# Optimization experiments

Measured on AMD Instinct MI355X. Metric: run time of the kernel, lower is better.

## Reference

```python
import jax, jax.numpy as jnp
import numpy as np

QUERY_DIM, FEAT_DIM, HID_DIM, OUT_DIM = 512, 2048, 512, 512
B, L, S, T = 8, 128, 100, 100


def setup_inputs() -> dict:
    key = jax.random.key(0)
    ks = jax.random.split(key, 9)
    d = {
        "query": jax.random.normal(ks[0], (B, L, QUERY_DIM), jnp.float32),
        "src": jax.random.normal(ks[1], (B, S, FEAT_DIM), jnp.float32),
        "trg": jax.random.normal(ks[2], (B, T, FEAT_DIM), jnp.float32),
        # params (LinearAct == Linear + identity act); src/trg projections share weights
        "Wq": jax.random.normal(ks[3], (QUERY_DIM, HID_DIM), jnp.float32) / np.sqrt(QUERY_DIM),
        "bq": jnp.zeros((HID_DIM,), jnp.float32),
        "Ws": jax.random.normal(ks[4], (FEAT_DIM, HID_DIM), jnp.float32) / np.sqrt(FEAT_DIM),
        "bs": jnp.zeros((HID_DIM,), jnp.float32),
        "Wo": jax.random.normal(ks[5], (HID_DIM + QUERY_DIM, OUT_DIM), jnp.float32) / np.sqrt(HID_DIM + QUERY_DIM),
        "bo": jnp.zeros((OUT_DIM,), jnp.float32),
    }
    return d


def reference(query, src, trg, Wq, bq, Ws, bs, Wo, bo):
    b, l, _ = query.shape
    s = src.shape[1]
    t = trg.shape[1]
    q = query @ Wq + bq          # b,l,k
    s_key = src @ Ws + bs        # b,s,k
    t_key = trg @ Ws + bs        # b,t,k
    hid = q.shape[-1]
    # score[b,l,s,t] = q . (s_key - t_key)/sqrt(2) / sqrt(hid) -- decomposed, no b,s,t,k tensor
    qs = jnp.einsum('blk,bsk->bls', q, s_key)
    qt = jnp.einsum('blk,btk->blt', q, t_key)
    score = (qs[:, :, :, None] - qt[:, :, None, :]) / jnp.sqrt(jnp.asarray(2.0 * hid, q.dtype))
    w = jax.nn.softmax(score.reshape(b, l, s * t), axis=-1).reshape(b, l, s, t)
    # ctx = sum_{s,t} w * (s_key - t_key)/sqrt(2), decomposed via marginals
    ws = w.sum(axis=3)           # b,l,s
    wt = w.sum(axis=2)           # b,l,t
    ctx = (jnp.einsum('bls,bsk->blk', ws, s_key) - jnp.einsum('blt,btk->blk', wt, t_key)) / jnp.sqrt(jnp.asarray(2.0, q.dtype))
    x = jnp.concatenate([query, ctx], axis=-1) @ Wo + bo
    return x
```

## Files before the change

### kernel.cpp

```cpp
#include <hip/hip_runtime.h>
#include <math.h>


typedef __attribute__((ext_vector_type(8))) short s16x8;
typedef __attribute__((ext_vector_type(4))) float f32x4;

__device__ __forceinline__ unsigned short f2bf(float f) {
    unsigned int u = __float_as_uint(f);
    return (unsigned short)((u + 0x7fffu + ((u >> 16) & 1u)) >> 16);
}

__device__ __forceinline__ s16x8 cvt8(const float* p) {
    float4 u = *(const float4*)p, w = *(const float4*)(p + 4);
    s16x8 o;
    o[0] = (short)f2bf(u.x); o[1] = (short)f2bf(u.y);
    o[2] = (short)f2bf(u.z); o[3] = (short)f2bf(u.w);
    o[4] = (short)f2bf(w.x); o[5] = (short)f2bf(w.y);
    o[6] = (short)f2bf(w.z); o[7] = (short)f2bf(w.w);
    return o;
}

__global__ __launch_bounds__(256) void k_prep(
    const float* __restrict__ Wq, const float* __restrict__ Ws,
    const float* __restrict__ Wo, const float* __restrict__ bs,
    unsigned short* __restrict__ WqT, unsigned short* __restrict__ WsT,
    unsigned short* __restrict__ WoT, float* __restrict__ keys) {
    __shared__ float tile[32][33];
    const int bid = blockIdx.x, t = threadIdx.x;

    if (bid < 1792) {
        const int id = bid;
        const float* W; unsigned short* O; int K, tk, tn;
        if (id < 256)       { W = Wq; O = WqT; K = 512;  tk = id >> 4;          tn = id & 15; }
        else if (id < 1280) { W = Ws; O = WsT; K = 2048; tk = (id - 256) >> 4;  tn = (id - 256) & 15; }
        else                { W = Wo; O = WoT; K = 1024; tk = (id - 1280) >> 4; tn = (id - 1280) & 15; }
        const int row = t >> 3, c4 = (t & 7) * 4;
        float4 v = *(const float4*)(W + (size_t)(tk * 32 + row) * 512 + tn * 32 + c4);
        tile[row][c4 + 0] = v.x; tile[row][c4 + 1] = v.y;
        tile[row][c4 + 2] = v.z; tile[row][c4 + 3] = v.w;
        __syncthreads();
        ushort4 o = make_ushort4(f2bf(tile[c4 + 0][row]), f2bf(tile[c4 + 1][row]),
                                 f2bf(tile[c4 + 2][row]), f2bf(tile[c4 + 3][row]));
        *(ushort4*)(O + (size_t)(tn * 32 + row) * K + tk * 32 + c4) = o;
    } else {
        const int f = ((bid - 1792) * 256 + t) * 4;
        *(float4*)(keys + f) = *(const float4*)(bs + (f & 511));
    }
}

__device__ __forceinline__ void gemm64_keys(
    const float* __restrict__ src, const float* __restrict__ trg,
    const unsigned short* __restrict__ BT, float* __restrict__ C,
    int m0, int n0, int kbase, unsigned short* As, unsigned short* Bs) {
    const int t = threadIdx.x;
    const int lane = t & 63, wid = t >> 6;
    const int wm = (wid & 1) * 32, wn = (wid >> 1) * 32;
    const int lr = lane & 15, lq = lane >> 4;
    const int r = t >> 3, c8 = (t & 7) * 8;

    const int ra_row = m0 + r, rb_row = m0 + r + 32;
    const float* arp = (ra_row < 800) ? (src + (size_t)ra_row * 2048)
                                      : (trg + (size_t)(ra_row - 800) * 2048);
    const float* brp = (rb_row < 800) ? (src + (size_t)rb_row * 2048)
                                      : (trg + (size_t)(rb_row - 800) * 2048);

    s16x8 ra0, ra1, rb0, rb1;
#define LDK(kt)                                                            \
    ra0 = cvt8(arp + (kt) + c8);                                           \
    ra1 = cvt8(brp + (kt) + c8);                                           \
    rb0 = *(const s16x8*)(BT + (size_t)(n0 + r)      * 2048 + (kt) + c8);  \
    rb1 = *(const s16x8*)(BT + (size_t)(n0 + r + 32) * 2048 + (kt) + c8);

    f32x4 acc[2][2] = {};
    LDK(kbase);
    for (int it = 0; it < 16; it++) {
        __syncthreads();
        *(s16x8*)&As[r * 72 + c8]        = ra0;
        *(s16x8*)&As[(r + 32) * 72 + c8] = ra1;
        *(s16x8*)&Bs[r * 72 + c8]        = rb0;
        *(s16x8*)&Bs[(r + 32) * 72 + c8] = rb1;
        __syncthreads();
        if (it < 15) { LDK(kbase + (it + 1) * 64); }
#pragma unroll
        for (int s = 0; s < 2; s++) {
            s16x8 a0 = *(const s16x8*)&As[(wm + lr) * 72      + s * 32 + lq * 8];
            s16x8 a1 = *(const s16x8*)&As[(wm + 16 + lr) * 72 + s * 32 + lq * 8];
            s16x8 b0 = *(const s16x8*)&Bs[(wn + lr) * 72      + s * 32 + lq * 8];
            s16x8 b1 = *(const s16x8*)&Bs[(wn + 16 + lr) * 72 + s * 32 + lq * 8];
            acc[0][0] = __builtin_amdgcn_mfma_f32_16x16x32_bf16(a0, b0, acc[0][0], 0, 0, 0);
            acc[0][1] = __builtin_amdgcn_mfma_f32_16x16x32_bf16(a0, b1, acc[0][1], 0, 0, 0);
            acc[1][0] = __builtin_amdgcn_mfma_f32_16x16x32_bf16(a1, b0, acc[1][0], 0, 0, 0);
            acc[1][1] = __builtin_amdgcn_mfma_f32_16x16x32_bf16(a1, b1, acc[1][1], 0, 0, 0);
        }
    }
#undef LDK
#pragma unroll
    for (int i = 0; i < 2; i++)
#pragma unroll
        for (int j = 0; j < 2; j++) {
            const int col = n0 + wn + j * 16 + lr;
            const int row = m0 + wm + i * 16 + lq * 4;
#pragma unroll
            for (int rr = 0; rr < 4; rr++)
                unsafeAtomicAdd(&C[(size_t)(row + rr) * 512 + col], acc[i][j][rr]);
        }
}

template <int MODE, bool AF32>
__device__ __forceinline__ void gemm32(
    const void* __restrict__ Av, const unsigned short* __restrict__ BT,
    const float* __restrict__ bias, void* __restrict__ Cv,
    int m0, int n0, int KA, int KB, int N, int kbase, int kiters,
    unsigned short* As, unsigned short* Bs) {
    const int t = threadIdx.x;
    const int lane = t & 63, wid = t >> 6;
    const int wm = (wid & 1) * 16, wn = (wid >> 1) * 32;
    const int lr = lane & 15, lq = lane >> 4;
    const int r = t >> 3, c8 = (t & 7) * 8;
    const float* Af = (const float*)Av;
    const unsigned short* Ab = (const unsigned short*)Av;

    s16x8 ra, rb0, rb1;
#define LD32(kt)                                                                 \
    ra  = AF32 ? cvt8(Af + (size_t)(m0 + r) * KA + (kt) + c8)                    \
               : *(const s16x8*)(Ab + (size_t)(m0 + r) * KA + (kt) + c8);        \
    rb0 = *(const s16x8*)(BT + (size_t)(n0 + r)      * KB + (kt) + c8);          \
    rb1 = *(const s16x8*)(BT + (size_t)(n0 + r + 32) * KB + (kt) + c8);

    f32x4 acc[2] = {};
    LD32(kbase);
    for (int it = 0; it < kiters; it++) {
        __syncthreads();
        *(s16x8*)&As[r * 72 + c8]        = ra;
        *(s16x8*)&Bs[r * 72 + c8]        = rb0;
        *(s16x8*)&Bs[(r + 32) * 72 + c8] = rb1;
        __syncthreads();
        if (it + 1 < kiters) { LD32(kbase + (it + 1) * 64); }
#pragma unroll
        for (int s = 0; s < 2; s++) {
            s16x8 a0 = *(const s16x8*)&As[(wm + lr) * 72      + s * 32 + lq * 8];
            s16x8 b0 = *(const s16x8*)&Bs[(wn + lr) * 72      + s * 32 + lq * 8];
            s16x8 b1 = *(const s16x8*)&Bs[(wn + 16 + lr) * 72 + s * 32 + lq * 8];
            acc[0] = __builtin_amdgcn_mfma_f32_16x16x32_bf16(a0, b0, acc[0], 0, 0, 0);
            acc[1] = __builtin_amdgcn_mfma_f32_16x16x32_bf16(a0, b1, acc[1], 0, 0, 0);
        }
    }
#undef LD32
#pragma unroll
    for (int j = 0; j < 2; j++) {
        const int col = n0 + wn + j * 16 + lr;
        const int row = m0 + wm + lq * 4;
        if (MODE == 1) {
            float* C = (float*)Cv;
#pragma unroll
            for (int rr = 0; rr < 4; rr++)
                unsafeAtomicAdd(&C[(size_t)(row + rr) * N + col], acc[j][rr]);
        } else if (MODE == 0) {
            float* C = (float*)Cv;
            const float bv = bias[col];
#pragma unroll
            for (int rr = 0; rr < 4; rr++)
                C[(size_t)(row + rr) * N + col] = acc[j][rr] + bv;
        } else {
            unsigned short* C = (unsigned short*)Cv;
            const float bv = bias[col];
#pragma unroll
            for (int rr = 0; rr < 4; rr++)
                C[(size_t)(row + rr) * N + col] = f2bf(acc[j][rr] + bv);
        }
    }
}

__global__ __launch_bounds__(256) void k_stageB(
    const float* __restrict__ query, const float* __restrict__ src,
    const float* __restrict__ trg, const unsigned short* __restrict__ WqT,
    const unsigned short* __restrict__ WsT, const unsigned short* __restrict__ WoT,
    const float* __restrict__ bq, const float* __restrict__ bo,
    unsigned short* __restrict__ qh, float* __restrict__ keys,
    float* __restrict__ out) {
    __shared__ __align__(16) unsigned short As[64 * 72];
    __shared__ __align__(16) unsigned short Bs[64 * 72];
    const int bid = blockIdx.x;
    if (bid < 400) {
        const int c = bid / 200, rem = bid % 200;
        const int mt = rem >> 3, nt = rem & 7;
        gemm64_keys(src, trg, WsT, keys, mt * 64, nt * 64, c * 1024, As, Bs);
    } else if (bid < 656) {
        const int r = bid - 400;
        const int mt = r >> 3, nt = r & 7;
        gemm32<2, true>(query, WqT, bq, qh, mt * 32, nt * 64, 512, 512, 512,
                        0, 8, As, Bs);
    } else {
        const int r = bid - 656;
        const int mt = r >> 3, nt = r & 7;
        gemm32<0, true>(query, WoT, bo, out, mt * 32, nt * 64, 512, 1024, 512,
                        0, 8, As, Bs);
    }
}

__global__ __launch_bounds__(256) void k_scgemm(
    const unsigned short* __restrict__ qh, const float* __restrict__ keys,
    float* __restrict__ sc) {
    __shared__ __align__(16) unsigned short As[32 * 72];
    __shared__ __align__(16) unsigned short Bs[64 * 72];
    const int bid = blockIdx.x;
    const int mt = bid >> 2, nt = bid & 3;
    const int m0 = mt * 32, b = mt >> 2, n0 = nt * 64;
    const int t = threadIdx.x;
    const int lane = t & 63, wid = t >> 6;
    const int wm = (wid & 1) * 16, wn = (wid >> 1) * 32;
    const int lr = lane & 15, lq = lane >> 4;
    const int r = t >> 3, c8 = (t & 7) * 8;

    const int nA = n0 + r, nB = n0 + r + 32;
    int kr0 = (nA < 128) ? (b * 100 + nA) : (800 + b * 100 + (nA - 128));
    int kr1 = (nB < 128) ? (b * 100 + nB) : (800 + b * 100 + (nB - 128));
    kr0 = kr0 > 1599 ? 1599 : kr0;
    kr1 = kr1 > 1599 ? 1599 : kr1;

    s16x8 ra, rb0, rb1;
#define LDSC(kt)                                                    \
    ra  = *(const s16x8*)(qh + (size_t)(m0 + r) * 512 + (kt) + c8); \
    rb0 = cvt8(keys + (size_t)kr0 * 512 + (kt) + c8);               \
    rb1 = cvt8(keys + (size_t)kr1 * 512 + (kt) + c8);

    f32x4 acc[2] = {};
    LDSC(0);
    for (int it = 0; it < 8; it++) {
        __syncthreads();
        *(s16x8*)&As[r * 72 + c8]        = ra;
        *(s16x8*)&Bs[r * 72 + c8]        = rb0;
        *(s16x8*)&Bs[(r + 32) * 72 + c8] = rb1;
        __syncthreads();
        if (it < 7) { LDSC((it + 1) * 64); }
#pragma unroll
        for (int s = 0; s < 2; s++) {
            s16x8 a0 = *(const s16x8*)&As[(wm + lr) * 72      + s * 32 + lq * 8];
            s16x8 b0 = *(const s16x8*)&Bs[(wn + lr) * 72      + s * 32 + lq * 8];
            s16x8 b1 = *(const s16x8*)&Bs[(wn + 16 + lr) * 72 + s * 32 + lq * 8];
            acc[0] = __builtin_amdgcn_mfma_f32_16x16x32_bf16(a0, b0, acc[0], 0, 0, 0);
            acc[1] = __builtin_amdgcn_mfma_f32_16x16x32_bf16(a0, b1, acc[1], 0, 0, 0);
        }
    }
#undef LDSC
#pragma unroll
    for (int j = 0; j < 2; j++) {
        const int col = n0 + wn + j * 16 + lr;
        const int row = m0 + wm + lq * 4;
        const float scale = (col >= 128) ? -(1.0f / 32.0f) : (1.0f / 32.0f);
#pragma unroll
        for (int rr = 0; rr < 4; rr++)
            sc[(size_t)(row + rr) * 256 + col] = acc[j][rr] * scale;
    }
}

__global__ __launch_bounds__(256) void k_ctx(
    const float* __restrict__ sc, const float* __restrict__ keys,
    unsigned short* __restrict__ ctxbf) {
    __shared__ float wbuf[200 * 33];
    __shared__ float Bs[40 * 32];

    const int t = threadIdx.x;
    const int b = blockIdx.y;
    const int n0 = blockIdx.x * 32;
    const int l0 = blockIdx.z * 32;
    const int wave = t >> 6, lane = t & 63;

    for (int i = 0; i < 8; i++) {
        const int li = wave * 8 + i;
        const float4 v = *(const float4*)(
            sc + (size_t)(b * 128 + l0 + li) * 256 + lane * 4);
        const float vv[4] = {v.x, v.y, v.z, v.w};
        const int c0 = lane * 4;
        float mS = -1e30f, mT = -1e30f;
#pragma unroll
        for (int j = 0; j < 4; j++) {
            const int col = c0 + j;
            if (col < 100) mS = fmaxf(mS, vv[j]);
            if (col >= 128 && col < 228) mT = fmaxf(mT, vv[j]);
        }
#pragma unroll
        for (int off = 32; off > 0; off >>= 1) {
            mS = fmaxf(mS, __shfl_xor(mS, off));
            mT = fmaxf(mT, __shfl_xor(mT, off));
        }
        float eS[4], eT[4], sS = 0.f, sT = 0.f;
#pragma unroll
        for (int j = 0; j < 4; j++) {
            const int col = c0 + j;
            eS[j] = (col < 100) ? __expf(vv[j] - mS) : 0.f;
            eT[j] = (col >= 128 && col < 228) ? __expf(vv[j] - mT) : 0.f;
            sS += eS[j]; sT += eT[j];
        }
#pragma unroll
        for (int off = 32; off > 0; off >>= 1) {
            sS += __shfl_xor(sS, off);
            sT += __shfl_xor(sT, off);
        }
        const float iS = 1.f / sS, iT = 1.f / sT;
#pragma unroll
        for (int j = 0; j < 4; j++) {
            const int col = c0 + j;
            if (col < 100) wbuf[col * 33 + li] = eS[j] * iS;
            if (col >= 128 && col < 228)
                wbuf[(100 + col - 128) * 33 + li] = eT[j] * iT;
        }
    }
    __syncthreads();

    const int tx = t & 7, ty = t >> 3;
    float rB[5];
    auto loadB = [&](int kbase) {
#pragma unroll
        for (int e = 0; e < 5; e++) {
            const int idx = t + e * 256;
            const int k = idx >> 5, j = idx & 31;
            const int kk = kbase + k;
            rB[e] = (kk < 100)
                ?  keys[(size_t)(b * 100 + kk) * 512 + n0 + j]
                : -keys[(size_t)(800 + b * 100 + (kk - 100)) * 512 + n0 + j];
        }
    };

    float acc[4] = {};
    loadB(0);
    for (int c5 = 0; c5 < 5; c5++) {
        __syncthreads();
#pragma unroll
        for (int e = 0; e < 5; e++) {
            const int idx = t + e * 256;
            Bs[idx] = rB[e];
        }
        __syncthreads();
        if (c5 < 4) loadB((c5 + 1) * 40);
#pragma unroll 8
        for (int k = 0; k < 40; k++) {
            const float ar = wbuf[(c5 * 40 + k) * 33 + ty];
            float br[4];
            *(float4*)br = *(const float4*)&Bs[k * 32 + tx * 4];
#pragma unroll
            for (int j = 0; j < 4; j++) acc[j] = fmaf(ar, br[j], acc[j]);
        }
    }

    const float s2 = 0.70710678118654752f;
    const int m = b * 128 + l0 + ty;
    ushort4 o = make_ushort4(f2bf(acc[0] * s2), f2bf(acc[1] * s2),
                             f2bf(acc[2] * s2), f2bf(acc[3] * s2));
    *(ushort4*)(ctxbf + (size_t)m * 512 + n0 + tx * 4) = o;
}

__global__ __launch_bounds__(256) void k_out(
    const unsigned short* __restrict__ ctxbf,
    const unsigned short* __restrict__ wotBot,
    float* __restrict__ out) {
    __shared__ __align__(16) unsigned short As[64 * 72];
    __shared__ __align__(16) unsigned short Bs[64 * 72];
    const int bid = blockIdx.x;
    const int mt = bid >> 3, nt = bid & 7;
    gemm32<1, false>(ctxbf, wotBot, nullptr, out, mt * 32, nt * 64,
                     512, 1024, 512, 0, 8, As, Bs);
}


extern "C" void kernel_launch(void* const* d_in, const int* in_sizes, int n_in,
                              void* d_out, int out_size, void* d_ws, size_t ws_size,
                              hipStream_t stream) {
    const float* query = (const float*)d_in[0];
    const float* src   = (const float*)d_in[1];
    const float* trg   = (const float*)d_in[2];
    const float* Wq    = (const float*)d_in[3];
    const float* bq    = (const float*)d_in[4];
    const float* Ws    = (const float*)d_in[5];
    const float* bs    = (const float*)d_in[6];
    const float* Wo    = (const float*)d_in[7];
    const float* bo    = (const float*)d_in[8];
    float* out = (float*)d_out;

    float* keys = (float*)d_ws;
    float* sc   = keys + 819200;
    unsigned short* qh    = (unsigned short*)(sc + 262144);
    unsigned short* ctxbf = qh    + 524288;
    unsigned short* wqt   = ctxbf + 524288;
    unsigned short* wst   = wqt   + 262144;
    unsigned short* wot   = wst   + 1048576;

    k_prep<<<2592, 256, 0, stream>>>(Wq, Ws, Wo, bs, wqt, wst, wot, keys);
    k_stageB<<<912, 256, 0, stream>>>(query, src, trg, wqt, wst, wot, bq, bo,
                                      qh, keys, out);
    k_scgemm<<<128, 256, 0, stream>>>(qh, keys, sc);
    k_ctx<<<dim3(16, 8, 4), 256, 0, stream>>>(sc, keys, ctxbf);
    k_out<<<256, 256, 0, stream>>>(ctxbf, wot + 512, out);
}
```

Measured before the change: 134.1 us.

## Reassociate context projection through Wo and fold output GEMM into context kernel

The key bias is dropped because it cancels in both the score difference and the weighted context difference. Since each marginal weight sums to one, ctx @ Wo_bot is rewritten as the weighted marginals times P = keys @ Wo_bot. P is computed in a new GEMM path that runs in the same launch as the score GEMM. The context kernel then atomically adds its result straight into the output, which removes the bf16 ctx buffer and the final k_out launch. In exchange, the larger P GEMM replaces the ctx-to-out GEMM, and the context kernel now issues fp32 atomics to the output.

```diff
diff --git a/kernel.cpp b/kernel.cpp
--- a/kernel.cpp
+++ b/kernel.cpp
@@ -22,7 +22,7 @@
 
 __global__ __launch_bounds__(256) void k_prep(
     const float* __restrict__ Wq, const float* __restrict__ Ws,
-    const float* __restrict__ Wo, const float* __restrict__ bs,
+    const float* __restrict__ Wo,
     unsigned short* __restrict__ WqT, unsigned short* __restrict__ WsT,
     unsigned short* __restrict__ WoT, float* __restrict__ keys) {
     __shared__ float tile[32][33];
@@ -44,7 +44,7 @@
         *(ushort4*)(O + (size_t)(tn * 32 + row) * K + tk * 32 + c4) = o;
     } else {
         const int f = ((bid - 1792) * 256 + t) * 4;
-        *(float4*)(keys + f) = *(const float4*)(bs + (f & 511));
+        *(float4*)(keys + f) = make_float4(0.f, 0.f, 0.f, 0.f);
     }
 }
 
@@ -106,36 +106,85 @@
         }
 }
 
-template <int MODE, bool AF32>
+__device__ __forceinline__ void gemm64_P(
+    const float* __restrict__ keys, const unsigned short* __restrict__ wotBot,
+    float* __restrict__ P, int m0, int n0, unsigned short* As,
+    unsigned short* Bs) {
+    const int t = threadIdx.x;
+    const int lane = t & 63, wid = t >> 6;
+    const int wm = (wid & 1) * 32, wn = (wid >> 1) * 32;
+    const int lr = lane & 15, lq = lane >> 4;
+    const int r = t >> 3, c8 = (t & 7) * 8;
+
+    s16x8 ra0, ra1, rb0, rb1;
+#define LDP(kt)                                                               \
+    ra0 = cvt8(keys + (size_t)(m0 + r)      * 512 + (kt) + c8);               \
+    ra1 = cvt8(keys + (size_t)(m0 + r + 32) * 512 + (kt) + c8);               \
+    rb0 = *(const s16x8*)(wotBot + (size_t)(n0 + r)      * 1024 + (kt) + c8); \
+    rb1 = *(const s16x8*)(wotBot + (size_t)(n0 + r + 32) * 1024 + (kt) + c8);
+
+    f32x4 acc[2][2] = {};
+    LDP(0);
+    for (int it = 0; it < 8; it++) {
+        __syncthreads();
+        *(s16x8*)&As[r * 72 + c8]        = ra0;
+        *(s16x8*)&As[(r + 32) * 72 + c8] = ra1;
+        *(s16x8*)&Bs[r * 72 + c8]        = rb0;
+        *(s16x8*)&Bs[(r + 32) * 72 + c8] = rb1;
+        __syncthreads();
+        if (it < 7) { LDP((it + 1) * 64); }
+#pragma unroll
+        for (int s = 0; s < 2; s++) {
+            s16x8 a0 = *(const s16x8*)&As[(wm + lr) * 72      + s * 32 + lq * 8];
+            s16x8 a1 = *(const s16x8*)&As[(wm + 16 + lr) * 72 + s * 32 + lq * 8];
+            s16x8 b0 = *(const s16x8*)&Bs[(wn + lr) * 72      + s * 32 + lq * 8];
+            s16x8 b1 = *(const s16x8*)&Bs[(wn + 16 + lr) * 72 + s * 32 + lq * 8];
+            acc[0][0] = __builtin_amdgcn_mfma_f32_16x16x32_bf16(a0, b0, acc[0][0], 0, 0, 0);
+            acc[0][1] = __builtin_amdgcn_mfma_f32_16x16x32_bf16(a0, b1, acc[0][1], 0, 0, 0);
+            acc[1][0] = __builtin_amdgcn_mfma_f32_16x16x32_bf16(a1, b0, acc[1][0], 0, 0, 0);
+            acc[1][1] = __builtin_amdgcn_mfma_f32_16x16x32_bf16(a1, b1, acc[1][1], 0, 0, 0);
+        }
+    }
+#undef LDP
+#pragma unroll
+    for (int i = 0; i < 2; i++)
+#pragma unroll
+        for (int j = 0; j < 2; j++) {
+            const int col = n0 + wn + j * 16 + lr;
+            const int row = m0 + wm + i * 16 + lq * 4;
+#pragma unroll
+            for (int rr = 0; rr < 4; rr++)
+                P[(size_t)(row + rr) * 512 + col] = acc[i][j][rr];
+        }
+}
+
+template <int MODE>
 __device__ __forceinline__ void gemm32(
-    const void* __restrict__ Av, const unsigned short* __restrict__ BT,
+    const float* __restrict__ A, const unsigned short* __restrict__ BT,
     const float* __restrict__ bias, void* __restrict__ Cv,
-    int m0, int n0, int KA, int KB, int N, int kbase, int kiters,
+    int m0, int n0, int KA, int KB, int N, int kiters,
     unsigned short* As, unsigned short* Bs) {
     const int t = threadIdx.x;
     const int lane = t & 63, wid = t >> 6;
     const int wm = (wid & 1) * 16, wn = (wid >> 1) * 32;
     const int lr = lane & 15, lq = lane >> 4;
     const int r = t >> 3, c8 = (t & 7) * 8;
-    const float* Af = (const float*)Av;
-    const unsigned short* Ab = (const unsigned short*)Av;
 
     s16x8 ra, rb0, rb1;
-#define LD32(kt)                                                                 \
-    ra  = AF32 ? cvt8(Af + (size_t)(m0 + r) * KA + (kt) + c8)                    \
-               : *(const s16x8*)(Ab + (size_t)(m0 + r) * KA + (kt) + c8);        \
-    rb0 = *(const s16x8*)(BT + (size_t)(n0 + r)      * KB + (kt) + c8);          \
+#define LD32(kt)                                                            \
+    ra  = cvt8(A + (size_t)(m0 + r) * KA + (kt) + c8);                      \
+    rb0 = *(const s16x8*)(BT + (size_t)(n0 + r)      * KB + (kt) + c8);     \
     rb1 = *(const s16x8*)(BT + (size_t)(n0 + r + 32) * KB + (kt) + c8);
 
     f32x4 acc[2] = {};
-    LD32(kbase);
+    LD32(0);
     for (int it = 0; it < kiters; it++) {
         __syncthreads();
         *(s16x8*)&As[r * 72 + c8]        = ra;
         *(s16x8*)&Bs[r * 72 + c8]        = rb0;
         *(s16x8*)&Bs[(r + 32) * 72 + c8] = rb1;
         __syncthreads();
-        if (it + 1 < kiters) { LD32(kbase + (it + 1) * 64); }
+        if (it + 1 < kiters) { LD32((it + 1) * 64); }
 #pragma unroll
         for (int s = 0; s < 2; s++) {
             s16x8 a0 = *(const s16x8*)&As[(wm + lr) * 72      + s * 32 + lq * 8];
@@ -150,20 +199,14 @@
     for (int j = 0; j < 2; j++) {
         const int col = n0 + wn + j * 16 + lr;
         const int row = m0 + wm + lq * 4;
-        if (MODE == 1) {
+        const float bv = bias[col];
+        if (MODE == 0) {
             float* C = (float*)Cv;
-#pragma unroll
-            for (int rr = 0; rr < 4; rr++)
-                unsafeAtomicAdd(&C[(size_t)(row + rr) * N + col], acc[j][rr]);
-        } else if (MODE == 0) {
-            float* C = (float*)Cv;
-            const float bv = bias[col];
 #pragma unroll
             for (int rr = 0; rr < 4; rr++)
                 C[(size_t)(row + rr) * N + col] = acc[j][rr] + bv;
         } else {
             unsigned short* C = (unsigned short*)Cv;
-            const float bv = bias[col];
 #pragma unroll
             for (int rr = 0; rr < 4; rr++)
                 C[(size_t)(row + rr) * N + col] = f2bf(acc[j][rr] + bv);
@@ -188,25 +231,33 @@
     } else if (bid < 656) {
         const int r = bid - 400;
         const int mt = r >> 3, nt = r & 7;
-        gemm32<2, true>(query, WqT, bq, qh, mt * 32, nt * 64, 512, 512, 512,
-                        0, 8, As, Bs);
+        gemm32<2>(query, WqT, bq, qh, mt * 32, nt * 64, 512, 512, 512,
+                  8, As, Bs);
     } else {
         const int r = bid - 656;
         const int mt = r >> 3, nt = r & 7;
-        gemm32<0, true>(query, WoT, bo, out, mt * 32, nt * 64, 512, 1024, 512,
-                        0, 8, As, Bs);
-    }
-}
-
-__global__ __launch_bounds__(256) void k_scgemm(
+        gemm32<0>(query, WoT, bo, out, mt * 32, nt * 64, 512, 1024, 512,
+                  8, As, Bs);
+    }
+}
+
+__global__ __launch_bounds__(256) void k_stageC(
     const unsigned short* __restrict__ qh, const float* __restrict__ keys,
-    float* __restrict__ sc) {
-    __shared__ __align__(16) unsigned short As[32 * 72];
+    const unsigned short* __restrict__ wotBot, float* __restrict__ sc,
+    float* __restrict__ P) {
+    __shared__ __align__(16) unsigned short As[64 * 72];
     __shared__ __align__(16) unsigned short Bs[64 * 72];
     const int bid = blockIdx.x;
+    const int t = threadIdx.x;
+
+    if (bid >= 128) {
+        const int rem = bid - 128;
+        gemm64_P(keys, wotBot, P, (rem >> 3) * 64, (rem & 7) * 64, As, Bs);
+        return;
+    }
+
     const int mt = bid >> 2, nt = bid & 3;
     const int m0 = mt * 32, b = mt >> 2, n0 = nt * 64;
-    const int t = threadIdx.x;
     const int lane = t & 63, wid = t >> 6;
     const int wm = (wid & 1) * 16, wn = (wid >> 1) * 32;
     const int lr = lane & 15, lq = lane >> 4;
@@ -254,9 +305,9 @@
     }
 }
 
-__global__ __launch_bounds__(256) void k_ctx(
-    const float* __restrict__ sc, const float* __restrict__ keys,
-    unsigned short* __restrict__ ctxbf) {
+__global__ __launch_bounds__(256) void k_stageD(
+    const float* __restrict__ sc, const float* __restrict__ P,
+    float* __restrict__ out) {
     __shared__ float wbuf[200 * 33];
     __shared__ float Bs[40 * 32];
 
@@ -317,8 +368,8 @@
             const int k = idx >> 5, j = idx & 31;
             const int kk = kbase + k;
             rB[e] = (kk < 100)
-                ?  keys[(size_t)(b * 100 + kk) * 512 + n0 + j]
-                : -keys[(size_t)(800 + b * 100 + (kk - 100)) * 512 + n0 + j];
+                ?  P[(size_t)(b * 100 + kk) * 512 + n0 + j]
+                : -P[(size_t)(800 + b * 100 + (kk - 100)) * 512 + n0 + j];
         }
     };
 
@@ -345,21 +396,9 @@
 
     const float s2 = 0.70710678118654752f;
     const int m = b * 128 + l0 + ty;
-    ushort4 o = make_ushort4(f2bf(acc[0] * s2), f2bf(acc[1] * s2),
-                             f2bf(acc[2] * s2), f2bf(acc[3] * s2));
-    *(ushort4*)(ctxbf + (size_t)m * 512 + n0 + tx * 4) = o;
-}
-
-__global__ __launch_bounds__(256) void k_out(
-    const unsigned short* __restrict__ ctxbf,
-    const unsigned short* __restrict__ wotBot,
-    float* __restrict__ out) {
-    __shared__ __align__(16) unsigned short As[64 * 72];
-    __shared__ __align__(16) unsigned short Bs[64 * 72];
-    const int bid = blockIdx.x;
-    const int mt = bid >> 3, nt = bid & 7;
-    gemm32<1, false>(ctxbf, wotBot, nullptr, out, mt * 32, nt * 64,
-                     512, 1024, 512, 0, 8, As, Bs);
+#pragma unroll
+    for (int j = 0; j < 4; j++)
+        unsafeAtomicAdd(&out[(size_t)m * 512 + n0 + tx * 4 + j], acc[j] * s2);
 }
 
 
@@ -372,23 +411,21 @@
     const float* Wq    = (const float*)d_in[3];
     const float* bq    = (const float*)d_in[4];
     const float* Ws    = (const float*)d_in[5];
-    const float* bs    = (const float*)d_in[6];
     const float* Wo    = (const float*)d_in[7];
     const float* bo    = (const float*)d_in[8];
     float* out = (float*)d_out;
 
     float* keys = (float*)d_ws;
     float* sc   = keys + 819200;
-    unsigned short* qh    = (unsigned short*)(sc + 262144);
-    unsigned short* ctxbf = qh    + 524288;
-    unsigned short* wqt   = ctxbf + 524288;
-    unsigned short* wst   = wqt   + 262144;
-    unsigned short* wot   = wst   + 1048576;
-
-    k_prep<<<2592, 256, 0, stream>>>(Wq, Ws, Wo, bs, wqt, wst, wot, keys);
+    float* P    = sc   + 262144;
+    unsigned short* qh  = (unsigned short*)(P + 819200);
+    unsigned short* wqt = qh  + 524288;
+    unsigned short* wst = wqt + 262144;
+    unsigned short* wot = wst + 1048576;
+
+    k_prep<<<2592, 256, 0, stream>>>(Wq, Ws, Wo, wqt, wst, wot, keys);
     k_stageB<<<912, 256, 0, stream>>>(query, src, trg, wqt, wst, wot, bq, bo,
                                       qh, keys, out);
-    k_scgemm<<<128, 256, 0, stream>>>(qh, keys, sc);
-    k_ctx<<<dim3(16, 8, 4), 256, 0, stream>>>(sc, keys, ctxbf);
-    k_out<<<256, 256, 0, stream>>>(ctxbf, wot + 512, out);
-}
+    k_stageC<<<328, 256, 0, stream>>>(qh, keys, wot + 512, sc, P);
+    k_stageD<<<dim3(16, 8, 4), 256, 0, stream>>>(sc, P, out);
+}
```

Measured after the change: 130.7 us, median of 2. -2.5%, faster.
